# Optimization experiments

Hardware: AMD Instinct MI355X
Metric: run time of the kernel (lower is better)

The kernel has to match this reference:

```python
import jax, jax.numpy as jnp
import numpy as np

B, S, H, QKV, NH, MLP = 4, 2048, 512, 512, 8, 2048
HD = QKV // NH
EPS = 1e-6


def _layernorm(x):
    # LayerNorm over last dim, no affine, eps=1e-6
    mu = jnp.mean(x, axis=-1, keepdims=True)
    var = jnp.mean(jnp.square(x - mu), axis=-1, keepdims=True)
    return (x - mu) * jax.lax.rsqrt(var + EPS)


def setup_inputs() -> dict:
    key = jax.random.key(0)
    ks = jax.random.split(key, 8)
    sc_in = 1.0 / np.sqrt(H)
    sc_qkv = 1.0 / np.sqrt(QKV)
    sc_mlp = 1.0 / np.sqrt(MLP)
    return {
        "input": jax.random.normal(ks[0], (B, S, H), dtype=jnp.float32),
        "mask": jnp.ones((B, S), dtype=jnp.float32),
        "Wq": jax.random.normal(ks[1], (H, QKV), dtype=jnp.float32) * sc_in,
        "Wk": jax.random.normal(ks[2], (H, QKV), dtype=jnp.float32) * sc_in,
        "Wv": jax.random.normal(ks[3], (H, QKV), dtype=jnp.float32) * sc_in,
        "Wo": jax.random.normal(ks[4], (QKV, H), dtype=jnp.float32) * sc_qkv,
        "W1": jax.random.normal(ks[5], (H, MLP), dtype=jnp.float32) * sc_in,
        "W2": jax.random.normal(ks[6], (MLP, H), dtype=jnp.float32) * sc_mlp,
    }


def reference(input, mask, Wq, Wk, Wv, Wo, W1, W2):
    # pre-mask + pre-norm
    x = input * mask[..., None]
    x = _layernorm(x)
    # qkv projections, split heads: [B,S,QKV] -> [B,NH,S,HD]
    def heads(t):
        return t.reshape(B, S, NH, HD).transpose(0, 2, 1, 3)
    q = heads(x @ Wq) * (1.0 / np.sqrt(HD))
    k = heads(x @ Wk)
    v = heads(x @ Wv)
    logits = jnp.einsum("bhqd,bhkd->bhqk", q, k)  # [B,NH,S,S]
    amask = mask[:, None, :, None]  # 'b q -> b 1 q 1'
    logits = logits + (-100000.0) * (1.0 - amask)
    att = jax.nn.softmax(logits, axis=-1)
    out = jnp.einsum("bhqk,bhkd->bhqd", att, v)
    out = out.transpose(0, 2, 1, 3).reshape(B, S, QKV)
    x = input + out @ Wo  # residual
    x = x * mask[..., None]
    y = _layernorm(x)
    ffn = jax.nn.gelu(y @ W1, approximate=False) @ W2
    return ffn + x
```

## Files before the change

### kernel.cpp

```cpp
#include <hip/hip_runtime.h>
#include <hip/hip_bf16.h>
#include <cmath>

typedef __attribute__((ext_vector_type(8))) short bf16x8;
typedef __attribute__((ext_vector_type(4))) short u16x4;
typedef __attribute__((ext_vector_type(4))) float f32x4;
typedef __attribute__((ext_vector_type(16))) float f32x16;
typedef unsigned short u16;
typedef unsigned int u32;

#define B_ 4
#define S_ 2048
#define H_ 512
#define NH_ 8
#define HD_ 64
#define MLP_ 2048
#define M_ (B_*S_)
#define LOG2E 1.44269504088896340736f

__device__ __forceinline__ float bf2f(u16 u){ u32 v=((u32)u)<<16; float f; __builtin_memcpy(&f,&v,4); return f; }
__device__ __forceinline__ u16 f2bf(float f){ u32 u; __builtin_memcpy(&u,&f,4); u32 r=(u+0x7fffu+((u>>16)&1u))>>16; return (u16)r; }
__device__ __forceinline__ u32 pk2(float lo, float hi2){
  __hip_bfloat162 t = __float22bfloat162_rn(make_float2(lo, hi2));
  u32 r; __builtin_memcpy(&r, &t, 4); return r;
}

__device__ __forceinline__ float xhalf_add(float x){
  float a = x, b = x;
  asm volatile("v_permlane32_swap_b32 %0, %1" : "+v"(a), "+v"(b));
  return a + b;
}

__device__ __forceinline__ float gelu_fast(float x){
  float arg = 2.30221265f*x + 0.10295034f*x*x*x;
  arg = fminf(fmaxf(arg, -30.0f), 30.0f);
  float e = __builtin_amdgcn_exp2f(arg);
  return x * e * __builtin_amdgcn_rcpf(1.0f + e);
}

__device__ __forceinline__ void gl16(const u16* g, u16* l) {
  __builtin_amdgcn_global_load_lds((const __attribute__((address_space(1))) u32*)(g),
                                   (__attribute__((address_space(3))) u32*)(l), 16, 0, 0);
}

__device__ __forceinline__ void swz_mn(int* mt, int* nt) {
  int lin = blockIdx.x + 64*blockIdx.y;
  int xcd = lin & 7, idx = lin >> 3;
  *mt = xcd*8 + (idx & 7);
  *nt = idx >> 3;
}

__device__ __forceinline__ void gemm_core(
    const u16* __restrict__ A, const u16* __restrict__ Bt,
    int lda, int ldb, int nkt, int m0, int n0,
    u16* As, u16* Bs, f32x4 (&acc)[4][4])
{
  const int tid = threadIdx.x;
  const int lane = tid & 63;
  const int w = tid >> 6;
  const int lr = lane & 15;
  const int g  = lane >> 4;
  const int wr = w >> 1, wc = w & 1;

  const int sr = lane >> 3;
  const int scol = ((lane & 7) ^ sr) << 3;

  int aoff[2][4], boff[2][4];
#pragma unroll
  for (int m = 0; m < 4; ++m) {
    int ra = wr*64 + m*16 + lr;
    int rb = wc*64 + m*16 + lr;
#pragma unroll
    for (int kk = 0; kk < 2; ++kk) {
      aoff[kk][m] = ra*64 + (((kk*4+g) ^ (ra&7))<<3);
      boff[kk][m] = rb*64 + (((kk*4+g) ^ (rb&7))<<3);
    }
  }
  const u16* Ap = A + (size_t)m0*lda;
  const u16* Bp = Bt + (size_t)n0*ldb;

#pragma unroll
  for (int c = 0; c < 4; ++c) {
    gl16(Ap + (size_t)(w*32 + c*8 + sr)*lda + scol, As + w*2048 + c*512);
    gl16(Bp + (size_t)(w*32 + c*8 + sr)*ldb + scol, Bs + w*2048 + c*512);
  }

  for (int kt = 0; kt < nkt; ++kt) {
    const int cb = (kt & 1) * 8192;
    if (kt + 1 < nkt) {
      const int k0 = (kt + 1) << 6;
      const int nb = ((kt + 1) & 1) * 8192;
#pragma unroll
      for (int c = 0; c < 4; ++c) {
        gl16(Ap + (size_t)(w*32 + c*8 + sr)*lda + k0 + scol, As + nb + w*2048 + c*512);
        gl16(Bp + (size_t)(w*32 + c*8 + sr)*ldb + k0 + scol, Bs + nb + w*2048 + c*512);
      }
      asm volatile("s_waitcnt vmcnt(8)" ::: "memory");
    } else {
      asm volatile("s_waitcnt vmcnt(0)" ::: "memory");
    }
    __builtin_amdgcn_s_barrier();

#pragma unroll
    for (int kk = 0; kk < 2; ++kk) {
      bf16x8 af[4], bfr[4];
#pragma unroll
      for (int m = 0; m < 4; ++m) {
        af[m]  = *(const bf16x8*)(As + cb + aoff[kk][m]);
        bfr[m] = *(const bf16x8*)(Bs + cb + boff[kk][m]);
      }
#pragma unroll
      for (int m = 0; m < 4; ++m) {
#pragma unroll
        for (int n = 0; n < 4; ++n) {
          acc[m][n] = __builtin_amdgcn_mfma_f32_16x16x32_bf16(af[m], bfr[n], acc[m][n], 0, 0, 0);
        }
      }
    }
    __builtin_amdgcn_s_barrier();
  }
}

__device__ __forceinline__ void gemm_core64(
    const u16* __restrict__ A, const u16* __restrict__ Bt,
    int lda, int ldb, int nkt, int m0, int n0,
    u16* As, u16* Bs, f32x4 (&acc)[2][4])
{
  const int tid = threadIdx.x;
  const int lane = tid & 63;
  const int w = tid >> 6;
  const int lr = lane & 15;
  const int g  = lane >> 4;

  const int sr = lane >> 3;
  const int scol = ((lane & 7) ^ sr) << 3;

  int aoff[2][2], boff[2][4];
#pragma unroll
  for (int m = 0; m < 2; ++m) {
    int ra = w*32 + m*16 + lr;
#pragma unroll
    for (int kk = 0; kk < 2; ++kk) aoff[kk][m] = ra*64 + (((kk*4+g) ^ (ra&7))<<3);
  }
#pragma unroll
  for (int n = 0; n < 4; ++n) {
    int rb = n*16 + lr;
#pragma unroll
    for (int kk = 0; kk < 2; ++kk) boff[kk][n] = rb*64 + (((kk*4+g) ^ (rb&7))<<3);
  }
  const u16* Ap = A + (size_t)m0*lda;
  const u16* Bp = Bt + (size_t)n0*ldb;

#pragma unroll
  for (int c = 0; c < 4; ++c)
    gl16(Ap + (size_t)(w*32 + c*8 + sr)*lda + scol, As + w*2048 + c*512);
#pragma unroll
  for (int c = 0; c < 2; ++c)
    gl16(Bp + (size_t)(w*16 + c*8 + sr)*ldb + scol, Bs + w*1024 + c*512);

  for (int kt = 0; kt < nkt; ++kt) {
    const int cbA = (kt & 1) * 8192;
    const int cbB = (kt & 1) * 4096;
    if (kt + 1 < nkt) {
      const int k0 = (kt + 1) << 6;
      const int nbA = ((kt + 1) & 1) * 8192;
      const int nbB = ((kt + 1) & 1) * 4096;
#pragma unroll
      for (int c = 0; c < 4; ++c)
        gl16(Ap + (size_t)(w*32 + c*8 + sr)*lda + k0 + scol, As + nbA + w*2048 + c*512);
#pragma unroll
      for (int c = 0; c < 2; ++c)
        gl16(Bp + (size_t)(w*16 + c*8 + sr)*ldb + k0 + scol, Bs + nbB + w*1024 + c*512);
      asm volatile("s_waitcnt vmcnt(6)" ::: "memory");
    } else {
      asm volatile("s_waitcnt vmcnt(0)" ::: "memory");
    }
    __builtin_amdgcn_s_barrier();

#pragma unroll
    for (int kk = 0; kk < 2; ++kk) {
      bf16x8 af[2], bfr[4];
#pragma unroll
      for (int m = 0; m < 2; ++m) af[m] = *(const bf16x8*)(As + cbA + aoff[kk][m]);
#pragma unroll
      for (int n = 0; n < 4; ++n) bfr[n] = *(const bf16x8*)(Bs + cbB + boff[kk][n]);
#pragma unroll
      for (int m = 0; m < 2; ++m) {
#pragma unroll
        for (int n = 0; n < 4; ++n) {
          acc[m][n] = __builtin_amdgcn_mfma_f32_16x16x32_bf16(af[m], bfr[n], acc[m][n], 0, 0, 0);
        }
      }
    }
    __builtin_amdgcn_s_barrier();
  }
}

__global__ __launch_bounds__(256,2) void k_qkv(
    const u16* __restrict__ xn, const u16* __restrict__ wqt,
    const u16* __restrict__ wkt, const u16* __restrict__ wvt,
    u16* __restrict__ q, u16* __restrict__ k, u16* __restrict__ vt)
{
  __shared__ u16 As[2*128*64], Bs[2*128*64];
  int mt, nt; swz_mn(&mt, &nt);
  int m0 = mt*128;
  int sel = nt >> 2;
  int n0 = (nt & 3)*128;
  const u16* Bt = sel==0 ? wqt : (sel==1 ? wkt : wvt);
  float alpha = (sel==0) ? 0.125f*LOG2E : 1.0f;
  f32x4 acc[4][4] = {};
  gemm_core(xn, Bt, H_, H_, H_/64, m0, n0, As, Bs, acc);
  const int lane = threadIdx.x&63, w = threadIdx.x>>6;
  const int lr = lane&15, g = lane>>4, wr = w>>1, wc = w&1;
  if (sel == 2) {
#pragma unroll
    for (int m=0;m<4;++m) {
#pragma unroll
      for (int n=0;n<4;++n) {
        int rowb = m0 + wr*64 + m*16 + g*4;
        int col  = n0 + wc*64 + n*16 + lr;
        int b = rowb >> 11, s = rowb & 2047;
        int h = col >> 6, d = col & 63;
        u16x4 t;
#pragma unroll
        for (int r=0;r<4;++r) t[r] = (short)f2bf(acc[m][n][r]);
        *(u16x4*)(vt + ((size_t)((b*NH_ + h)*HD_ + d))*S_ + s) = t;
      }
    }
  } else {
    u16* O = sel==0 ? q : k;
#pragma unroll
    for (int m=0;m<4;++m) {
#pragma unroll
      for (int n=0;n<4;++n) {
#pragma unroll
        for (int r=0;r<4;++r) {
          int row = m0 + wr*64 + m*16 + g*4 + r;
          int col = n0 + wc*64 + n*16 + lr;
          O[(size_t)row*H_ + col] = f2bf(acc[m][n][r]*alpha);
        }
      }
    }
  }
}

template<int EPI>
__global__ __launch_bounds__(256,2) void k_gemm(
    const u16* __restrict__ A, const u16* __restrict__ Bt, void* __restrict__ Ov,
    const void* __restrict__ aux, const float* __restrict__ maskv,
    int N, int K)
{
  __shared__ u16 As[2*128*64], Bs[2*128*64];
  int mt, nt; swz_mn(&mt, &nt);
  int m0 = mt*128, n0 = nt*128;
  f32x4 acc[4][4] = {};
  gemm_core(A, Bt, K, K, K>>6, m0, n0, As, Bs, acc);
  const int lane = threadIdx.x&63, w = threadIdx.x>>6;
  const int lr = lane&15, g = lane>>4, wr = w>>1, wc = w&1;
#pragma unroll
  for (int m=0;m<4;++m) {
#pragma unroll
    for (int n=0;n<4;++n) {
#pragma unroll
      for (int r=0;r<4;++r) {
        int row = m0 + wr*64 + m*16 + g*4 + r;
        int col = n0 + wc*64 + n*16 + lr;
        float val = acc[m][n][r];
        if (EPI == 1) {
          ((u16*)Ov)[(size_t)row*N + col] = f2bf(gelu_fast(val));
        }
      }
    }
  }
}

template<int EPI>
__global__ __launch_bounds__(256,3) void k_gemm64(
    const u16* __restrict__ A, const u16* __restrict__ Bt, void* __restrict__ Ov,
    const void* __restrict__ aux, const float* __restrict__ maskv,
    int N, int K)
{
  __shared__ u16 As[2*128*64], Bs[2*64*64];
  int mt, nt; swz_mn(&mt, &nt);
  int m0 = mt*128, n0 = nt*64;
  f32x4 acc[2][4] = {};
  gemm_core64(A, Bt, K, K, K>>6, m0, n0, As, Bs, acc);
  const int lane = threadIdx.x&63, w = threadIdx.x>>6;
  const int lr = lane&15, g = lane>>4;
#pragma unroll
  for (int m=0;m<2;++m) {
#pragma unroll
    for (int n=0;n<4;++n) {
#pragma unroll
      for (int r=0;r<4;++r) {
        int row = m0 + w*32 + m*16 + g*4 + r;
        int col = n0 + n*16 + lr;
        float val = acc[m][n][r];
        if (EPI == 2) {
          float mv = maskv[row];
          val = (((const float*)aux)[(size_t)row*N + col] + val)*mv;
          ((u16*)Ov)[(size_t)row*N + col] = f2bf(val);
        } else if (EPI == 3) {
          val += bf2f(((const u16*)aux)[(size_t)row*N + col]);
          ((float*)Ov)[(size_t)row*N + col] = val;
        }
      }
    }
  }
}

__global__ __launch_bounds__(256) void k_lnb(const u16* __restrict__ in,
    u16* __restrict__ out)
{
  int row = blockIdx.x*4 + (threadIdx.x>>6);
  int lane = threadIdx.x & 63;
  bf16x8 d = *(const bf16x8*)(in + (size_t)row*H_ + lane*8);
  float x[8]; float s = 0.f, s2 = 0.f;
#pragma unroll
  for (int j=0;j<8;++j){ x[j] = bf2f((u16)d[j]); s += x[j]; s2 += x[j]*x[j]; }
#pragma unroll
  for (int m=1;m<32;m<<=1){ s += __shfl_xor(s,m); s2 += __shfl_xor(s2,m); }
  s = xhalf_add(s); s2 = xhalf_add(s2);
  float mu = s*(1.0f/H_);
  float var = s2*(1.0f/H_) - mu*mu;
  float inv = rsqrtf(var + 1e-6f);
  bf16x8 o;
#pragma unroll
  for (int j=0;j<8;++j) o[j] = (short)f2bf((x[j]-mu)*inv);
  *(bf16x8*)(out + (size_t)row*H_ + lane*8) = o;
}

__global__ __launch_bounds__(256) void k_pre(
    const float* __restrict__ Wq, const float* __restrict__ Wk,
    const float* __restrict__ Wv, const float* __restrict__ Wo,
    const float* __restrict__ W1, const float* __restrict__ W2,
    u16* __restrict__ wqt, u16* __restrict__ wkt, u16* __restrict__ wvt,
    u16* __restrict__ wot, u16* __restrict__ w1t, u16* __restrict__ w2t,
    const float* __restrict__ input, const float* __restrict__ mask,
    u16* __restrict__ xn)
{
  __shared__ u16 t[32][33];
  const int id = blockIdx.x;
  const int tx = threadIdx.x & 31, ty = threadIdx.x >> 5;

  if (id < 1024) {
    int z = id >> 8, tt = id & 255;
    const float* src = z==0?Wq : z==1?Wk : z==2?Wv : Wo;
    u16* dst = z==0?wqt : z==1?wkt : z==2?wvt : wot;
    int c0 = (tt & 15)*32, r0 = (tt >> 4)*32;
#pragma unroll
    for (int i=0;i<32;i+=8) t[ty+i][tx] = f2bf(src[(size_t)(r0+ty+i)*512 + c0+tx]);
    __syncthreads();
#pragma unroll
    for (int i=0;i<32;i+=8) dst[(size_t)(c0+ty+i)*512 + r0+tx] = t[tx][ty+i];
  } else if (id < 3072) {
    int z = (id-1024) >> 10, tt = (id-1024) & 1023;
    const float* src = z ? W2 : W1;
    u16* dst = z ? w2t : w1t;
    int R = z ? 2048 : 512;
    int C = z ? 512 : 2048;
    int a = tt & 63, bq = tt >> 6;
    int c0 = (z ? bq : a)*32;
    int r0 = (z ? a : bq)*32;
#pragma unroll
    for (int i=0;i<32;i+=8) t[ty+i][tx] = f2bf(src[(size_t)(r0+ty+i)*C + c0+tx]);
    __syncthreads();
#pragma unroll
    for (int i=0;i<32;i+=8) dst[(size_t)(c0+ty+i)*R + r0+tx] = t[tx][ty+i];
  } else {
    int row = (id-3072)*4 + (threadIdx.x>>6);
    int lane = threadIdx.x & 63;
    const f32x4* p = (const f32x4*)(input + (size_t)row*H_ + lane*8);
    f32x4 a = p[0], b = p[1];
    float mv = mask[row];
    float x[8]; float s = 0.f, s2 = 0.f;
#pragma unroll
    for (int j=0;j<4;++j){ x[j] = a[j]*mv; x[4+j] = b[j]*mv; }
#pragma unroll
    for (int j=0;j<8;++j){ s += x[j]; s2 += x[j]*x[j]; }
#pragma unroll
    for (int m=1;m<32;m<<=1){ s += __shfl_xor(s,m); s2 += __shfl_xor(s2,m); }
    s = xhalf_add(s); s2 = xhalf_add(s2);
    float mu = s*(1.0f/H_);
    float var = s2*(1.0f/H_) - mu*mu;
    float inv = rsqrtf(var + 1e-6f);
    bf16x8 o;
#pragma unroll
    for (int j=0;j<8;++j) o[j] = (short)f2bf((x[j]-mu)*inv);
    *(bf16x8*)(xn + (size_t)row*H_ + lane*8) = o;
  }
}

__global__ __launch_bounds__(256) void k_attn(
    const u16* __restrict__ q, const u16* __restrict__ kmat,
    const u16* __restrict__ vt, const float* __restrict__ mask,
    u16* __restrict__ o)
{
  __shared__ u16 Ks[2][64*64];
  __shared__ u16 Vs[2][64*64];
  __shared__ float bias[S_];
  __shared__ float lsums[4][32];

  const int tid = threadIdx.x;
  const int lane = tid & 63;
  const int w = tid >> 6;
  const int l31 = lane & 31;
  const int hi = lane >> 5;
  const int bh = blockIdx.y, b = bh >> 3, h = bh & 7;
  const int q0 = blockIdx.x * 128;

  const int sr = lane >> 3;
  const int sl = (lane & 7) ^ (sr & 7);
  const u16* ks0 = kmat + (size_t)(b*S_ + w*16 + sr)*H_ + h*HD_ + sl*8;
  const u16* ks1 = ks0 + (size_t)8*H_;
  const u16* vs0 = vt + ((size_t)bh*HD_ + w*16 + sr)*S_ + sl*8;
  const u16* vs1 = vs0 + (size_t)8*S_;

  {
    u16* kd = &Ks[0][0] + w*1024;
    u16* vd = &Vs[0][0] + w*1024;
    gl16(ks0, kd); gl16(ks1, kd + 512);
    gl16(vs0, vd); gl16(vs1, vd + 512);
  }

  for (int j = tid; j < S_; j += 256) bias[j] = -144269.5f * (1.0f - mask[b*S_ + j]);

  bf16x8 qf[4];
  {
    const u16* qp = q + (size_t)(b*S_ + q0 + w*32 + l31)*H_ + h*HD_ + hi*8;
#pragma unroll
    for (int ds = 0; ds < 4; ++ds) qf[ds] = *(const bf16x8*)(qp + ds*16);
  }

  f32x16 po0 = {}, po1 = {};
  float mreg = -1e30f, lsum = 0.f;

  __syncthreads();

  for (int jt = 0; jt < 32; ++jt) {
    const int buf = jt & 1;
    if (jt < 31) {
      const int j0 = (jt + 1) * 64;
      u16* kd = &Ks[buf ^ 1][0] + w*1024;
      u16* vd = &Vs[buf ^ 1][0] + w*1024;
      gl16(ks0 + (size_t)j0*H_, kd); gl16(ks1 + (size_t)j0*H_, kd + 512);
      gl16(vs0 + j0, vd);            gl16(vs1 + j0, vd + 512);
      asm volatile("s_waitcnt vmcnt(4)" ::: "memory");
    } else {
      asm volatile("s_waitcnt vmcnt(0)" ::: "memory");
    }
    __builtin_amdgcn_s_barrier();

    const u16* kt  = &Ks[buf][0];
    const u16* vtl = &Vs[buf][0];

    f32x16 s0, s1;
    const float* bp = &bias[jt*64 + hi*4];
#pragma unroll
    for (int kb = 0; kb < 2; ++kb) {
      f32x16 acc;
#pragma unroll
      for (int g2 = 0; g2 < 4; ++g2) {
        f32x4 b4 = *(const f32x4*)(bp + kb*32 + g2*8);
        acc[g2*4+0] = b4[0]; acc[g2*4+1] = b4[1];
        acc[g2*4+2] = b4[2]; acc[g2*4+3] = b4[3];
      }
      const int key = kb*32 + l31;
      const u16* kr = kt + key*64;
      __builtin_amdgcn_s_setprio(1);
#pragma unroll
      for (int ds = 0; ds < 4; ++ds) {
        bf16x8 kf = *(const bf16x8*)(kr + (((ds*2 + hi) ^ (key & 7)) << 3));
        acc = __builtin_amdgcn_mfma_f32_32x32x16_bf16(kf, qf[ds], acc, 0, 0, 0);
      }
      __builtin_amdgcn_s_setprio(0);
      if (kb == 0) s0 = acc; else s1 = acc;
    }

    float mx = fmaxf(s0[0], s1[0]);
#pragma unroll
    for (int r = 1; r < 16; ++r) mx = fmaxf(fmaxf(s0[r], s1[r]), mx);
    mx = fmaxf(mx, __shfl_xor(mx, 32));
    if (__any(mx > mreg + 8.0f)) {
      float mn = fmaxf(mreg, mx);
      float sc = __builtin_amdgcn_exp2f(mreg - mn);
      lsum *= sc;
#pragma unroll
      for (int r = 0; r < 16; ++r) { po0[r] *= sc; po1[r] *= sc; }
      mreg = mn;
    }
    float ps = 0.f;
#pragma unroll
    for (int r = 0; r < 16; ++r) { float p = __builtin_amdgcn_exp2f(s0[r]-mreg); s0[r] = p; ps += p; }
#pragma unroll
    for (int r = 0; r < 16; ++r) { float p = __builtin_amdgcn_exp2f(s1[r]-mreg); s1[r] = p; ps += p; }
    ps += __shfl_xor(ps, 32);
    lsum += ps;

#pragma unroll
    for (int kb = 0; kb < 2; ++kb) {
      const f32x16& sv = kb ? s1 : s0;
      u32 w01 = pk2(sv[0],  sv[1]);
      u32 w23 = pk2(sv[2],  sv[3]);
      u32 w45 = pk2(sv[4],  sv[5]);
      u32 w67 = pk2(sv[6],  sv[7]);
      asm volatile("v_permlane32_swap_b32 %0, %1" : "+v"(w01), "+v"(w45));
      asm volatile("v_permlane32_swap_b32 %0, %1" : "+v"(w23), "+v"(w67));
      u32 w89 = pk2(sv[8],  sv[9]);
      u32 wab = pk2(sv[10], sv[11]);
      u32 wcd = pk2(sv[12], sv[13]);
      u32 wef = pk2(sv[14], sv[15]);
      asm volatile("v_permlane32_swap_b32 %0, %1" : "+v"(w89), "+v"(wcd));
      asm volatile("v_permlane32_swap_b32 %0, %1" : "+v"(wab), "+v"(wef));
      union { u32 wrd[4]; bf16x8 v; } f0, f1;
      f0.wrd[0]=w01; f0.wrd[1]=w23; f0.wrd[2]=w45; f0.wrd[3]=w67;
      f1.wrd[0]=w89; f1.wrd[1]=wab; f1.wrd[2]=wcd; f1.wrd[3]=wef;
      __builtin_amdgcn_s_setprio(1);
#pragma unroll
      for (int ks = 0; ks < 2; ++ks) {
        bf16x8 pa = ks ? f1.v : f0.v;
#pragma unroll
        for (int nb = 0; nb < 2; ++nb) {
          int dd = nb*32 + l31;
          int slot = ((kb*4 + ks*2 + hi) ^ (dd & 7)) << 3;
          bf16x8 vf = *(const bf16x8*)(vtl + dd*64 + slot);
          if (nb == 0) po0 = __builtin_amdgcn_mfma_f32_32x32x16_bf16(pa, vf, po0, 0,0,0);
          else         po1 = __builtin_amdgcn_mfma_f32_32x32x16_bf16(pa, vf, po1, 0,0,0);
        }
      }
      __builtin_amdgcn_s_setprio(0);
    }
    __builtin_amdgcn_s_barrier();
  }

  if (hi == 0) lsums[w][l31] = lsum;
  f32x4 li[4];
#pragma unroll
  for (int g2i = 0; g2i < 4; ++g2i) {
    f32x4 t = *(const f32x4*)&lsums[w][g2i*8 + hi*4];
    li[g2i][0] = 1.0f/t[0]; li[g2i][1] = 1.0f/t[1];
    li[g2i][2] = 1.0f/t[2]; li[g2i][3] = 1.0f/t[3];
  }
  u16* op = o + (size_t)(b*S_ + q0 + w*32)*H_ + h*HD_;
#pragma unroll
  for (int nb = 0; nb < 2; ++nb) {
#pragma unroll
    for (int r = 0; r < 16; ++r) {
      int row = (r&3) + 8*(r>>2) + 4*hi;
      float val = (nb ? po1[r] : po0[r]) * li[r>>2][r&3];
      op[(size_t)row*H_ + nb*32 + l31] = f2bf(val);
    }
  }
}

extern "C" void kernel_launch(void* const* d_in, const int* in_sizes, int n_in,
                              void* d_out, int out_size, void* d_ws, size_t ws_size,
                              hipStream_t stream) {
  const float* input = (const float*)d_in[0];
  const float* mask  = (const float*)d_in[1];
  const float* Wq = (const float*)d_in[2];
  const float* Wk = (const float*)d_in[3];
  const float* Wv = (const float*)d_in[4];
  const float* Wo = (const float*)d_in[5];
  const float* W1 = (const float*)d_in[6];
  const float* W2 = (const float*)d_in[7];
  float* out = (float*)d_out;
  u16* ws = (u16*)d_ws;

  u16* wqt = ws;
  u16* wkt = wqt + 262144;
  u16* wvt = wkt + 262144;
  u16* wot = wvt + 262144;
  u16* w1t = wot + 262144;
  u16* w2t = w1t + 1048576;
  u16* xn  = w2t + 1048576;
  u16* q   = xn  + 4194304;
  u16* k   = q   + 4194304;
  u16* v   = k   + 4194304;
  u16* vt  = v   + 4194304;
  u16*   attn = xn;
  u16*   x2b  = q;
  u16*   y    = v;
  u16*   h1   = vt;

  dim3 blk(256);
  k_pre<<<dim3(5120), blk, 0, stream>>>(Wq, Wk, Wv, Wo, W1, W2,
                                        wqt, wkt, wvt, wot, w1t, w2t,
                                        input, mask, xn);
  k_qkv<<<dim3(64,12), blk, 0, stream>>>(xn, wqt, wkt, wvt, q, k, vt);
  k_attn<<<dim3(16,32), blk, 0, stream>>>(q, k, vt, mask, attn);
  k_gemm64<2><<<dim3(64,8), blk, 0, stream>>>(attn, wot, (void*)x2b, (const void*)input, mask, 512, 512);
  k_lnb<<<2048, blk, 0, stream>>>(x2b, y);
  k_gemm<1><<<dim3(64,16), blk, 0, stream>>>(y, w1t, (void*)h1, nullptr, nullptr, 2048, 512);
  k_gemm64<3><<<dim3(64,8), blk, 0, stream>>>(h1, w2t, (void*)out, (const void*)x2b, nullptr, 512, 2048);
}
```

Before: 164.4 us.

## Fold second LayerNorm into O-proj epilogue stats and W1 GEMM epilogue

Removes the standalone LayerNorm kernel. The O-projection epilogue now accumulates per-row sum and sum-of-squares with atomics. The W1 GEMM consumes the un-normalized residual directly and applies the normalization algebraically using precomputed column sums of W1: inv*(acc - mu*colsum). This saves a kernel launch and a full read/write pass, at the cost of atomics, a serial column-sum loop in the prep kernel, and numerical differences because the matmul now runs on unnormalized bf16 values.

```diff
diff --git a/kernel.cpp b/kernel.cpp
--- a/kernel.cpp
+++ b/kernel.cpp
@@ -257,16 +257,24 @@
   gemm_core(A, Bt, K, K, K>>6, m0, n0, As, Bs, acc);
   const int lane = threadIdx.x&63, w = threadIdx.x>>6;
   const int lr = lane&15, g = lane>>4, wr = w>>1, wc = w&1;
-#pragma unroll
-  for (int m=0;m<4;++m) {
-#pragma unroll
-    for (int n=0;n<4;++n) {
+  if (EPI == 1) {
+    const float2* st = (const float2*)aux;
+    const float* cs1 = maskv;
+    float csv[4];
+#pragma unroll
+    for (int n=0;n<4;++n) csv[n] = cs1[n0 + wc*64 + n*16 + lr];
+#pragma unroll
+    for (int m=0;m<4;++m) {
 #pragma unroll
       for (int r=0;r<4;++r) {
         int row = m0 + wr*64 + m*16 + g*4 + r;
-        int col = n0 + wc*64 + n*16 + lr;
-        float val = acc[m][n][r];
-        if (EPI == 1) {
+        float2 t = st[row];
+        float mu = t.x*(1.0f/H_);
+        float inv = rsqrtf(t.y*(1.0f/H_) - mu*mu + 1e-6f);
+#pragma unroll
+        for (int n=0;n<4;++n) {
+          int col = n0 + wc*64 + n*16 + lr;
+          float val = inv*(acc[m][n][r] - mu*csv[n]);
           ((u16*)Ov)[(size_t)row*N + col] = f2bf(gelu_fast(val));
         }
       }
@@ -278,7 +286,7 @@
 __global__ __launch_bounds__(256,3) void k_gemm64(
     const u16* __restrict__ A, const u16* __restrict__ Bt, void* __restrict__ Ov,
     const void* __restrict__ aux, const float* __restrict__ maskv,
-    int N, int K)
+    int N, int K, float2* __restrict__ st)
 {
   __shared__ u16 As[2*128*64], Bs[2*64*64];
   int mt, nt; swz_mn(&mt, &nt);
@@ -287,47 +295,53 @@
   gemm_core64(A, Bt, K, K, K>>6, m0, n0, As, Bs, acc);
   const int lane = threadIdx.x&63, w = threadIdx.x>>6;
   const int lr = lane&15, g = lane>>4;
-#pragma unroll
-  for (int m=0;m<2;++m) {
-#pragma unroll
-    for (int n=0;n<4;++n) {
+  if (EPI == 2) {
+    float ss[2][4] = {{0,0,0,0},{0,0,0,0}};
+    float ss2[2][4] = {{0,0,0,0},{0,0,0,0}};
+#pragma unroll
+    for (int m=0;m<2;++m) {
 #pragma unroll
       for (int r=0;r<4;++r) {
         int row = m0 + w*32 + m*16 + g*4 + r;
-        int col = n0 + n*16 + lr;
-        float val = acc[m][n][r];
-        if (EPI == 2) {
-          float mv = maskv[row];
-          val = (((const float*)aux)[(size_t)row*N + col] + val)*mv;
+        float mv = maskv[row];
+#pragma unroll
+        for (int n=0;n<4;++n) {
+          int col = n0 + n*16 + lr;
+          float val = (((const float*)aux)[(size_t)row*N + col] + acc[m][n][r])*mv;
           ((u16*)Ov)[(size_t)row*N + col] = f2bf(val);
-        } else if (EPI == 3) {
-          val += bf2f(((const u16*)aux)[(size_t)row*N + col]);
+          ss[m][r] += val; ss2[m][r] += val*val;
+        }
+      }
+    }
+#pragma unroll
+    for (int m=0;m<2;++m) {
+#pragma unroll
+      for (int r=0;r<4;++r) {
+        float s = ss[m][r], s2v = ss2[m][r];
+#pragma unroll
+        for (int d=1; d<16; d<<=1){ s += __shfl_xor(s,d); s2v += __shfl_xor(s2v,d); }
+        if (lr == 0) {
+          int row = m0 + w*32 + m*16 + g*4 + r;
+          atomicAdd(&st[row].x, s);
+          atomicAdd(&st[row].y, s2v);
+        }
+      }
+    }
+  } else {
+#pragma unroll
+    for (int m=0;m<2;++m) {
+#pragma unroll
+      for (int n=0;n<4;++n) {
+#pragma unroll
+        for (int r=0;r<4;++r) {
+          int row = m0 + w*32 + m*16 + g*4 + r;
+          int col = n0 + n*16 + lr;
+          float val = acc[m][n][r] + bf2f(((const u16*)aux)[(size_t)row*N + col]);
           ((float*)Ov)[(size_t)row*N + col] = val;
         }
       }
     }
   }
-}
-
-__global__ __launch_bounds__(256) void k_lnb(const u16* __restrict__ in,
-    u16* __restrict__ out)
-{
-  int row = blockIdx.x*4 + (threadIdx.x>>6);
-  int lane = threadIdx.x & 63;
-  bf16x8 d = *(const bf16x8*)(in + (size_t)row*H_ + lane*8);
-  float x[8]; float s = 0.f, s2 = 0.f;
-#pragma unroll
-  for (int j=0;j<8;++j){ x[j] = bf2f((u16)d[j]); s += x[j]; s2 += x[j]*x[j]; }
-#pragma unroll
-  for (int m=1;m<32;m<<=1){ s += __shfl_xor(s,m); s2 += __shfl_xor(s2,m); }
-  s = xhalf_add(s); s2 = xhalf_add(s2);
-  float mu = s*(1.0f/H_);
-  float var = s2*(1.0f/H_) - mu*mu;
-  float inv = rsqrtf(var + 1e-6f);
-  bf16x8 o;
-#pragma unroll
-  for (int j=0;j<8;++j) o[j] = (short)f2bf((x[j]-mu)*inv);
-  *(bf16x8*)(out + (size_t)row*H_ + lane*8) = o;
 }
 
 __global__ __launch_bounds__(256) void k_pre(
@@ -337,7 +351,7 @@
     u16* __restrict__ wqt, u16* __restrict__ wkt, u16* __restrict__ wvt,
     u16* __restrict__ wot, u16* __restrict__ w1t, u16* __restrict__ w2t,
     const float* __restrict__ input, const float* __restrict__ mask,
-    u16* __restrict__ xn)
+    u16* __restrict__ xn, float2* __restrict__ st, float* __restrict__ cs1)
 {
   __shared__ u16 t[32][33];
   const int id = blockIdx.x;
@@ -367,7 +381,7 @@
     __syncthreads();
 #pragma unroll
     for (int i=0;i<32;i+=8) dst[(size_t)(c0+ty+i)*R + r0+tx] = t[tx][ty+i];
-  } else {
+  } else if (id < 5120) {
     int row = (id-3072)*4 + (threadIdx.x>>6);
     int lane = threadIdx.x & 63;
     const f32x4* p = (const f32x4*)(input + (size_t)row*H_ + lane*8);
@@ -388,6 +402,14 @@
 #pragma unroll
     for (int j=0;j<8;++j) o[j] = (short)f2bf((x[j]-mu)*inv);
     *(bf16x8*)(xn + (size_t)row*H_ + lane*8) = o;
+  } else if (id < 5136) {
+    f32x4 z4 = {0.f, 0.f, 0.f, 0.f};
+    ((f32x4*)st)[(id-5120)*256 + threadIdx.x] = z4;
+  } else {
+    int c = (id-5136)*256 + threadIdx.x;
+    float s = 0.f;
+    for (int k2 = 0; k2 < 512; ++k2) s += bf2f(f2bf(W1[(size_t)k2*MLP_ + c]));
+    cs1[c] = s;
   }
 }
 
@@ -580,17 +602,17 @@
   u16* vt  = v   + 4194304;
   u16*   attn = xn;
   u16*   x2b  = q;
-  u16*   y    = v;
   u16*   h1   = vt;
+  float2* st  = (float2*)v;
+  float*  cs1 = (float*)(st + 8192);
 
   dim3 blk(256);
-  k_pre<<<dim3(5120), blk, 0, stream>>>(Wq, Wk, Wv, Wo, W1, W2,
+  k_pre<<<dim3(5144), blk, 0, stream>>>(Wq, Wk, Wv, Wo, W1, W2,
                                         wqt, wkt, wvt, wot, w1t, w2t,
-                                        input, mask, xn);
+                                        input, mask, xn, st, cs1);
   k_qkv<<<dim3(64,12), blk, 0, stream>>>(xn, wqt, wkt, wvt, q, k, vt);
   k_attn<<<dim3(16,32), blk, 0, stream>>>(q, k, vt, mask, attn);
-  k_gemm64<2><<<dim3(64,8), blk, 0, stream>>>(attn, wot, (void*)x2b, (const void*)input, mask, 512, 512);
-  k_lnb<<<2048, blk, 0, stream>>>(x2b, y);
-  k_gemm<1><<<dim3(64,16), blk, 0, stream>>>(y, w1t, (void*)h1, nullptr, nullptr, 2048, 512);
-  k_gemm64<3><<<dim3(64,8), blk, 0, stream>>>(h1, w2t, (void*)out, (const void*)x2b, nullptr, 512, 2048);
-}
+  k_gemm64<2><<<dim3(64,8), blk, 0, stream>>>(attn, wot, (void*)x2b, (const void*)input, mask, 512, 512, st);
+  k_gemm<1><<<dim3(64,16), blk, 0, stream>>>(x2b, w1t, (void*)h1, (const void*)st, cs1, 2048, 512);
+  k_gemm64<3><<<dim3(64,8), blk, 0, stream>>>(h1, w2t, (void*)out, (const void*)x2b, nullptr, 512, 2048, nullptr);
+}
```

New measurement: 189.8 us. 1.15x slower.
